# Kernel optimization log

Measured on AMD Instinct MI355X. Metric: run time of the kernel, lower is better.

## Reference

```python
import jax, jax.numpy as jnp
import numpy as np

DECAY = 0.8  # voltage decay (init arg)

# ThresholdActivation: spike = (v > 0), straight-through surrogate gradient
@jax.custom_vjp
def spike(x):
    return (x > 0).astype(x.dtype)

def _spike_fwd(x):
    return (x > 0).astype(x.dtype), None

def _spike_bwd(res, g):
    return (g,)

spike.defvjp(_spike_fwd, _spike_bwd)


def setup_inputs() -> dict:
    key = jax.random.key(0)
    k1, k2, k3 = jax.random.split(key, 3)
    B, I, H, T = 128, 512, 512, 512
    x = jax.random.normal(k1, (B, I, T), dtype=jnp.float32)
    # torch: nn.init.normal_(w, 0.1, 0.1)
    W = 0.1 + 0.1 * jax.random.normal(k2, (I, H), dtype=jnp.float32)
    b = 0.1 + 0.1 * jax.random.normal(k3, (1, H), dtype=jnp.float32)
    return {"x": x, "W": W, "b": b}


def reference(x, W, b):
    # x: (B, I, T), W: (I, H), b: (1, H)
    B, I, T = x.shape
    H = W.shape[1]
    xt = jnp.transpose(x, (2, 0, 1))              # (T, B, I)
    xw = jnp.einsum('tbi,ih->tbh', xt, W)         # batch all input matmuls: (T, B, H)

    def step(carry, xw_t):
        h, y = carry
        # s_t = relu(Wx + decay * s_{t-1} * (1 - y_{t-1}))
        h = jax.nn.relu(xw_t + DECAY * h * (1.0 - y))
        # y_t = threshold(s_t + bias)
        y = spike(h + b)
        return (h, y), y

    init = (jnp.zeros((B, H), x.dtype), jnp.zeros((B, H), x.dtype))
    _, ys = jax.lax.scan(step, init, xw)          # ys: (T, B, H)
    outputs = jnp.transpose(ys, (1, 2, 0))        # (B, H, T)
    # SNU applies SpikeActivation to the concatenated outputs
    return spike(outputs)
```

## Files before the change

kernel.cpp:

```cpp
#include <hip/hip_runtime.h>


#define DECAYF 0.8f

__global__ __launch_bounds__(512) void compact_cols(const float* __restrict__ bias,
                                                    int* __restrict__ hdr,
                                                    int* __restrict__ idx) {
    __shared__ unsigned long long wmask[8];
    const int tid = threadIdx.x;
    const bool p = (bias[tid] <= 0.0f);
    unsigned long long m = __ballot(p);
    const int wid = tid >> 6, lane = tid & 63;
    if (lane == 0) wmask[wid] = m;
    __syncthreads();
    int before = 0, total = 0;
    #pragma unroll
    for (int w = 0; w < 8; w++) {
        int c = __popcll(wmask[w]);
        if (w < wid) before += c;
        total += c;
    }
    if (p) idx[before + __popcll(m & ((1ull << lane) - 1ull))] = tid;
    __syncthreads();
    int idx0 = (total > 0) ? idx[0] : 0;
    if (tid >= total && tid < 256) idx[tid] = idx0;
    if (tid == 0) {
        int pc = (total + 127) & ~127;
        if (pc > 256) pc = 256;
        hdr[0] = total;
        hdr[1] = pc;
    }
}

__global__ __launch_bounds__(256) void gather_W(const float* __restrict__ W,
                                                const int* __restrict__ idx,
                                                float* __restrict__ Wc) {
    const int i = blockIdx.x;
    const int j = threadIdx.x;
    Wc[i * 256 + j] = W[i * 512 + idx[j]];
}

__global__ __launch_bounds__(256) void fill_ones(const float* __restrict__ bias,
                                                 float4* __restrict__ out4) {
    const int f4 = blockIdx.x * 256 + threadIdx.x;
    const int h = (f4 >> 7) & 511;
    if (bias[h] > 0.0f) out4[f4] = make_float4(1.f, 1.f, 1.f, 1.f);
}

__global__ __launch_bounds__(256) void gemm_c(const float* __restrict__ x,
                                              const float* __restrict__ Wc,
                                              const int* __restrict__ hdr,
                                              float* __restrict__ xwc) {
    const int h0 = blockIdx.x * 128;
    if (h0 >= hdr[1]) return;
    const int Bn = 128, I = 512, T = 512;
    const int b  = blockIdx.z;
    const int t0 = blockIdx.y * 128;

    __shared__ float As[16][132];
    __shared__ float Bs[16][132];

    const int tid  = threadIdx.x;
    const int wave = tid >> 6;
    const int lane = tid & 63;
    const int lx = lane & 7;
    const int ly = lane >> 3;
    const int m_base = ((wave >> 1) << 6) + ly * 8;
    const int n_base = ((wave & 1) << 6) + lx * 8;

    float acc[8][8];
    #pragma unroll
    for (int i = 0; i < 8; i++)
        #pragma unroll
        for (int j = 0; j < 8; j++) acc[i][j] = 0.f;

    const float* xb = x + (size_t)b * I * T;

    for (int k0 = 0; k0 < I; k0 += 16) {
        #pragma unroll
        for (int j = 0; j < 2; j++) {
            int idx = tid + j * 256;
            int row = idx >> 5;
            int c4  = (idx & 31) << 2;
            *(float4*)&As[row][c4] = *(const float4*)(xb + (size_t)(k0 + row) * T + t0 + c4);
            *(float4*)&Bs[row][c4] = *(const float4*)(Wc + (size_t)(k0 + row) * 256 + h0 + c4);
        }
        __syncthreads();
        #pragma unroll
        for (int kk = 0; kk < 16; kk++) {
            float a[8], bb[8];
            *(float4*)&a[0]  = *(const float4*)&As[kk][m_base];
            *(float4*)&a[4]  = *(const float4*)&As[kk][m_base + 4];
            *(float4*)&bb[0] = *(const float4*)&Bs[kk][n_base];
            *(float4*)&bb[4] = *(const float4*)&Bs[kk][n_base + 4];
            #pragma unroll
            for (int mi = 0; mi < 8; mi++)
                #pragma unroll
                for (int ni = 0; ni < 8; ni++)
                    acc[mi][ni] = fmaf(a[mi], bb[ni], acc[mi][ni]);
        }
        __syncthreads();
    }

    #pragma unroll
    for (int mi = 0; mi < 8; mi++) {
        int t = t0 + m_base + mi;
        float* o = xwc + ((size_t)t * Bn + b) * 256 + h0 + n_base;
        *(float4*)o       = *(float4*)&acc[mi][0];
        *(float4*)(o + 4) = *(float4*)&acc[mi][4];
    }
}

__global__ __launch_bounds__(128) void snu_scan_c(const float* __restrict__ xwc,
                                                  const float* __restrict__ bias,
                                                  const int* __restrict__ hdr,
                                                  const int* __restrict__ idx,
                                                  float* __restrict__ out) {
    const int T = 512;
    const int count = hdr[0];
    const int jt = blockIdx.x >> 7;
    const int b  = blockIdx.x & 127;
    const int j  = jt * 128 + threadIdx.x;
    if (j >= count) return;
    const int h = idx[j];
    const float bv = bias[h];
    const float* p = xwc + (size_t)b * 256 + j;
    float* o = out + ((size_t)b * 512 + h) * (size_t)T;
    const size_t STR = (size_t)128 * 256;

    float hs = 0.f, y = 0.f;
    float buf[16], nxt[16], yb[16];
    #pragma unroll
    for (int q = 0; q < 16; q++) buf[q] = p[(size_t)q * STR];

    for (int t0 = 0; t0 < T; t0 += 16) {
        const bool more = (t0 + 16) < T;
        #pragma unroll
        for (int q = 0; q < 16; q++) nxt[q] = more ? p[(size_t)(t0 + 16 + q) * STR] : 0.f;
        #pragma unroll
        for (int q = 0; q < 16; q++) {
            hs = fmaf(DECAYF * hs, 1.f - y, buf[q]);
            hs = fmaxf(hs, 0.f);
            y  = (hs + bv > 0.f) ? 1.f : 0.f;
            yb[q] = y;
        }
        #pragma unroll
        for (int q = 0; q < 4; q++)
            *(float4*)(o + t0 + q * 4) = *(float4*)&yb[q * 4];
        #pragma unroll
        for (int q = 0; q < 16; q++) buf[q] = nxt[q];
    }
}

extern "C" void kernel_launch(void* const* d_in, const int* in_sizes, int n_in,
                              void* d_out, int out_size, void* d_ws, size_t ws_size,
                              hipStream_t stream) {
    const float* x    = (const float*)d_in[0];
    const float* W    = (const float*)d_in[1];
    const float* bias = (const float*)d_in[2];
    float* out = (float*)d_out;

    char* ws = (char*)d_ws;
    int*   hdr = (int*)(ws + 0);
    int*   idx = (int*)(ws + 64);
    float* Wc  = (float*)(ws + 4096);
    float* xwc = (float*)(ws + (1 << 20));

    compact_cols<<<1, 512, 0, stream>>>(bias, hdr, idx);
    gather_W<<<512, 256, 0, stream>>>(W, idx, Wc);
    fill_ones<<<32768, 256, 0, stream>>>(bias, (float4*)out);
    dim3 g1(2, 4, 128);
    gemm_c<<<g1, 256, 0, stream>>>(x, Wc, hdr, xwc);
    snu_scan_c<<<256, 128, 0, stream>>>(xwc, bias, hdr, idx, out);
}
```

Baseline: 402.4 us.

## Fuse ones-fill into scan kernel and shrink GEMM tile along time

Drops the separate fill_ones kernel. A new scan_fill kernel, one block per (128-column slice, batch), writes the constant-one rows for positive-bias columns and then runs the recurrent scan for the compacted columns through a column-to-compact-index map that compact_cols now also emits. The GEMM time tile goes from 128 to 64 and each thread's accumulator from 8x8 to 8x4, which doubles the grid and raises occupancy. The cost is more redundant W tile loads and a serial loop over 128 columns inside each scan block.

Result: no change. 400.1 us (-0.6%).

```diff
diff --git a/kernel.cpp b/kernel.cpp
--- a/kernel.cpp
+++ b/kernel.cpp
@@ -5,7 +5,8 @@
 
 __global__ __launch_bounds__(512) void compact_cols(const float* __restrict__ bias,
                                                     int* __restrict__ hdr,
-                                                    int* __restrict__ idx) {
+                                                    int* __restrict__ idx,
+                                                    int* __restrict__ jof) {
     __shared__ unsigned long long wmask[8];
     const int tid = threadIdx.x;
     const bool p = (bias[tid] <= 0.0f);
@@ -20,7 +21,9 @@
         if (w < wid) before += c;
         total += c;
     }
-    if (p) idx[before + __popcll(m & ((1ull << lane) - 1ull))] = tid;
+    const int rank = before + __popcll(m & ((1ull << lane) - 1ull));
+    if (p) idx[rank] = tid;
+    jof[tid] = p ? rank : -1;
     __syncthreads();
     int idx0 = (total > 0) ? idx[0] : 0;
     if (tid >= total && tid < 256) idx[tid] = idx0;
@@ -40,63 +43,55 @@
     Wc[i * 256 + j] = W[i * 512 + idx[j]];
 }
 
-__global__ __launch_bounds__(256) void fill_ones(const float* __restrict__ bias,
-                                                 float4* __restrict__ out4) {
-    const int f4 = blockIdx.x * 256 + threadIdx.x;
-    const int h = (f4 >> 7) & 511;
-    if (bias[h] > 0.0f) out4[f4] = make_float4(1.f, 1.f, 1.f, 1.f);
-}
-
 __global__ __launch_bounds__(256) void gemm_c(const float* __restrict__ x,
                                               const float* __restrict__ Wc,
                                               const int* __restrict__ hdr,
                                               float* __restrict__ xwc) {
     const int h0 = blockIdx.x * 128;
     if (h0 >= hdr[1]) return;
-    const int Bn = 128, I = 512, T = 512;
+    const int Bn = 128, I = 512, T = 512, NC = 256;
     const int b  = blockIdx.z;
-    const int t0 = blockIdx.y * 128;
+    const int t0 = blockIdx.y * 64;
 
-    __shared__ float As[16][132];
+    __shared__ float As[16][68];
     __shared__ float Bs[16][132];
 
-    const int tid  = threadIdx.x;
-    const int wave = tid >> 6;
-    const int lane = tid & 63;
-    const int lx = lane & 7;
-    const int ly = lane >> 3;
-    const int m_base = ((wave >> 1) << 6) + ly * 8;
-    const int n_base = ((wave & 1) << 6) + lx * 8;
+    const int tid = threadIdx.x;
+    const int tx = tid & 31;
+    const int ty = tid >> 5;
 
-    float acc[8][8];
+    float acc[8][4];
     #pragma unroll
     for (int i = 0; i < 8; i++)
         #pragma unroll
-        for (int j = 0; j < 8; j++) acc[i][j] = 0.f;
+        for (int j = 0; j < 4; j++) acc[i][j] = 0.f;
 
     const float* xb = x + (size_t)b * I * T;
 
     for (int k0 = 0; k0 < I; k0 += 16) {
+        {
+            int row = tid >> 4;
+            int c4  = (tid & 15) << 2;
+            *(float4*)&As[row][c4] = *(const float4*)(xb + (size_t)(k0 + row) * T + t0 + c4);
+        }
         #pragma unroll
         for (int j = 0; j < 2; j++) {
-            int idx = tid + j * 256;
-            int row = idx >> 5;
-            int c4  = (idx & 31) << 2;
-            *(float4*)&As[row][c4] = *(const float4*)(xb + (size_t)(k0 + row) * T + t0 + c4);
-            *(float4*)&Bs[row][c4] = *(const float4*)(Wc + (size_t)(k0 + row) * 256 + h0 + c4);
+            int id2 = tid + j * 256;
+            int row = id2 >> 5;
+            int c4  = (id2 & 31) << 2;
+            *(float4*)&Bs[row][c4] = *(const float4*)(Wc + (size_t)(k0 + row) * NC + h0 + c4);
         }
         __syncthreads();
         #pragma unroll
         for (int kk = 0; kk < 16; kk++) {
-            float a[8], bb[8];
-            *(float4*)&a[0]  = *(const float4*)&As[kk][m_base];
-            *(float4*)&a[4]  = *(const float4*)&As[kk][m_base + 4];
-            *(float4*)&bb[0] = *(const float4*)&Bs[kk][n_base];
-            *(float4*)&bb[4] = *(const float4*)&Bs[kk][n_base + 4];
+            float a[8], bb[4];
+            *(float4*)&a[0]  = *(const float4*)&As[kk][ty * 8];
+            *(float4*)&a[4]  = *(const float4*)&As[kk][ty * 8 + 4];
+            *(float4*)&bb[0] = *(const float4*)&Bs[kk][tx * 4];
             #pragma unroll
             for (int mi = 0; mi < 8; mi++)
                 #pragma unroll
-                for (int ni = 0; ni < 8; ni++)
+                for (int ni = 0; ni < 4; ni++)
                     acc[mi][ni] = fmaf(a[mi], bb[ni], acc[mi][ni]);
         }
         __syncthreads();
@@ -104,29 +99,40 @@
 
     #pragma unroll
     for (int mi = 0; mi < 8; mi++) {
-        int t = t0 + m_base + mi;
-        float* o = xwc + ((size_t)t * Bn + b) * 256 + h0 + n_base;
-        *(float4*)o       = *(float4*)&acc[mi][0];
-        *(float4*)(o + 4) = *(float4*)&acc[mi][4];
+        int t = t0 + ty * 8 + mi;
+        float* o = xwc + ((size_t)t * Bn + b) * NC + h0 + tx * 4;
+        *(float4*)o = *(float4*)&acc[mi][0];
     }
 }
 
-__global__ __launch_bounds__(128) void snu_scan_c(const float* __restrict__ xwc,
-                                                  const float* __restrict__ bias,
-                                                  const int* __restrict__ hdr,
-                                                  const int* __restrict__ idx,
-                                                  float* __restrict__ out) {
-    const int T = 512;
-    const int count = hdr[0];
-    const int jt = blockIdx.x >> 7;
-    const int b  = blockIdx.x & 127;
-    const int j  = jt * 128 + threadIdx.x;
-    if (j >= count) return;
-    const int h = idx[j];
-    const float bv = bias[h];
-    const float* p = xwc + (size_t)b * 256 + j;
-    float* o = out + ((size_t)b * 512 + h) * (size_t)T;
-    const size_t STR = (size_t)128 * 256;
+__global__ __launch_bounds__(128) void scan_fill(const float* __restrict__ xwc,
+                                                 const float* __restrict__ bias,
+                                                 const int* __restrict__ jof,
+                                                 float* __restrict__ out) {
+    const int T = 512, NC = 256;
+    const int ht  = blockIdx.x >> 7;
+    const int b   = blockIdx.x & 127;
+    const int tid = threadIdx.x;
+    const int hb  = ht * 128;
+
+    __shared__ unsigned char spos[128];
+    const float bv = bias[hb + tid];
+    spos[tid] = (bv > 0.0f) ? 1 : 0;
+    __syncthreads();
+
+    const float4 ones = make_float4(1.f, 1.f, 1.f, 1.f);
+    for (int hh = 0; hh < 128; hh++) {
+        if (spos[hh]) {
+            float4* o4 = (float4*)(out + ((size_t)b * 512 + hb + hh) * T);
+            o4[tid] = ones;
+        }
+    }
+
+    const int j = jof[hb + tid];
+    if (j < 0) return;
+    const float* p = xwc + (size_t)b * NC + j;
+    float* o = out + ((size_t)b * 512 + hb + tid) * (size_t)T;
+    const size_t STR = (size_t)128 * NC;
 
     float hs = 0.f, y = 0.f;
     float buf[16], nxt[16], yb[16];
@@ -163,13 +169,13 @@
     char* ws = (char*)d_ws;
     int*   hdr = (int*)(ws + 0);
     int*   idx = (int*)(ws + 64);
+    int*   jof = (int*)(ws + 2048);
     float* Wc  = (float*)(ws + 4096);
     float* xwc = (float*)(ws + (1 << 20));
 
-    compact_cols<<<1, 512, 0, stream>>>(bias, hdr, idx);
+    compact_cols<<<1, 512, 0, stream>>>(bias, hdr, idx, jof);
     gather_W<<<512, 256, 0, stream>>>(W, idx, Wc);
-    fill_ones<<<32768, 256, 0, stream>>>(bias, (float4*)out);
-    dim3 g1(2, 4, 128);
+    dim3 g1(2, 8, 128);
     gemm_c<<<g1, 256, 0, stream>>>(x, Wc, hdr, xwc);
-    snu_scan_c<<<256, 128, 0, stream>>>(xwc, bias, hdr, idx, out);
+    scan_fill<<<512, 128, 0, stream>>>(xwc, bias, jof, out);
 }
```

## Store GEMM output time-contiguous per column so scan reads vectorized rows

Applied to the files above, without the earlier changes.

The GEMM epilogue now writes its result as [b][column][t] instead of [t][b][column], so each scan thread reads its own time series contiguously with float4 loads. Before, each thread made strided scalar loads across time steps. The fill_ones kernel now writes eight float4s per thread with an eighth of the blocks, and it is launched after the GEMM. The GEMM stores now go out as scattered float4 writes along the column dimension, which may coalesce worse.

Result: slower. 448.2 us (+11.4%).

```diff
diff --git a/kernel.cpp b/kernel.cpp
--- a/kernel.cpp
+++ b/kernel.cpp
@@ -42,9 +42,14 @@
 
 __global__ __launch_bounds__(256) void fill_ones(const float* __restrict__ bias,
                                                  float4* __restrict__ out4) {
-    const int f4 = blockIdx.x * 256 + threadIdx.x;
-    const int h = (f4 >> 7) & 511;
-    if (bias[h] > 0.0f) out4[f4] = make_float4(1.f, 1.f, 1.f, 1.f);
+    const float4 ones = make_float4(1.f, 1.f, 1.f, 1.f);
+    const int base = blockIdx.x * 2048;
+    #pragma unroll
+    for (int q = 0; q < 8; q++) {
+        int f4 = base + q * 256 + threadIdx.x;
+        int h = (f4 >> 7) & 511;
+        if (bias[h] > 0.0f) out4[f4] = ones;
+    }
 }
 
 __global__ __launch_bounds__(256) void gemm_c(const float* __restrict__ x,
@@ -53,7 +58,7 @@
                                               float* __restrict__ xwc) {
     const int h0 = blockIdx.x * 128;
     if (h0 >= hdr[1]) return;
-    const int Bn = 128, I = 512, T = 512;
+    const int I = 512, T = 512, NC = 256;
     const int b  = blockIdx.z;
     const int t0 = blockIdx.y * 128;
 
@@ -79,11 +84,11 @@
     for (int k0 = 0; k0 < I; k0 += 16) {
         #pragma unroll
         for (int j = 0; j < 2; j++) {
-            int idx = tid + j * 256;
-            int row = idx >> 5;
-            int c4  = (idx & 31) << 2;
+            int id2 = tid + j * 256;
+            int row = id2 >> 5;
+            int c4  = (id2 & 31) << 2;
             *(float4*)&As[row][c4] = *(const float4*)(xb + (size_t)(k0 + row) * T + t0 + c4);
-            *(float4*)&Bs[row][c4] = *(const float4*)(Wc + (size_t)(k0 + row) * 256 + h0 + c4);
+            *(float4*)&Bs[row][c4] = *(const float4*)(Wc + (size_t)(k0 + row) * NC + h0 + c4);
         }
         __syncthreads();
         #pragma unroll
@@ -103,11 +108,12 @@
     }
 
     #pragma unroll
-    for (int mi = 0; mi < 8; mi++) {
-        int t = t0 + m_base + mi;
-        float* o = xwc + ((size_t)t * Bn + b) * 256 + h0 + n_base;
-        *(float4*)o       = *(float4*)&acc[mi][0];
-        *(float4*)(o + 4) = *(float4*)&acc[mi][4];
+    for (int ni = 0; ni < 8; ni++) {
+        float4 lo = make_float4(acc[0][ni], acc[1][ni], acc[2][ni], acc[3][ni]);
+        float4 hi = make_float4(acc[4][ni], acc[5][ni], acc[6][ni], acc[7][ni]);
+        float* o = xwc + ((size_t)b * NC + h0 + n_base + ni) * (size_t)T + t0 + m_base;
+        *(float4*)o       = lo;
+        *(float4*)(o + 4) = hi;
     }
 }
 
@@ -116,27 +122,30 @@
                                                   const int* __restrict__ hdr,
                                                   const int* __restrict__ idx,
                                                   float* __restrict__ out) {
-    const int T = 512;
+    const int T = 512, NC = 256;
     const int count = hdr[0];
+    const int b  = blockIdx.x & 127;
     const int jt = blockIdx.x >> 7;
-    const int b  = blockIdx.x & 127;
     const int j  = jt * 128 + threadIdx.x;
     if (j >= count) return;
     const int h = idx[j];
     const float bv = bias[h];
-    const float* p = xwc + (size_t)b * 256 + j;
+    const float4* p = (const float4*)(xwc + ((size_t)b * NC + j) * (size_t)T);
     float* o = out + ((size_t)b * 512 + h) * (size_t)T;
-    const size_t STR = (size_t)128 * 256;
 
     float hs = 0.f, y = 0.f;
-    float buf[16], nxt[16], yb[16];
+    float4 nx[4];
     #pragma unroll
-    for (int q = 0; q < 16; q++) buf[q] = p[(size_t)q * STR];
+    for (int q = 0; q < 4; q++) nx[q] = p[q];
 
     for (int t0 = 0; t0 < T; t0 += 16) {
+        float buf[16], yb[16];
+        #pragma unroll
+        for (int q = 0; q < 4; q++) *(float4*)&buf[q * 4] = nx[q];
         const bool more = (t0 + 16) < T;
         #pragma unroll
-        for (int q = 0; q < 16; q++) nxt[q] = more ? p[(size_t)(t0 + 16 + q) * STR] : 0.f;
+        for (int q = 0; q < 4; q++)
+            nx[q] = more ? p[(t0 >> 2) + 4 + q] : make_float4(0.f, 0.f, 0.f, 0.f);
         #pragma unroll
         for (int q = 0; q < 16; q++) {
             hs = fmaf(DECAYF * hs, 1.f - y, buf[q]);
@@ -147,8 +156,6 @@
         #pragma unroll
         for (int q = 0; q < 4; q++)
             *(float4*)(o + t0 + q * 4) = *(float4*)&yb[q * 4];
-        #pragma unroll
-        for (int q = 0; q < 16; q++) buf[q] = nxt[q];
     }
 }
 
@@ -168,8 +175,8 @@
 
     compact_cols<<<1, 512, 0, stream>>>(bias, hdr, idx);
     gather_W<<<512, 256, 0, stream>>>(W, idx, Wc);
-    fill_ones<<<32768, 256, 0, stream>>>(bias, (float4*)out);
     dim3 g1(2, 4, 128);
     gemm_c<<<g1, 256, 0, stream>>>(x, Wc, hdr, xwc);
+    fill_ones<<<4096, 256, 0, stream>>>(bias, (float4*)out);
     snu_scan_c<<<256, 128, 0, stream>>>(xwc, bias, hdr, idx, out);
 }
```
